# Performance work log

Measured on AMD Instinct MI355X. Metric: run time of the kernel, lower is better.

Reference implementation:

```python
import jax, jax.numpy as jnp
import numpy as np

B, S, E, H, D, RD = 1, 2048, 2560, 32, 80, 32  # batch, seq, n_embd, heads, head_dim, rotary_dim


def setup_inputs() -> dict:
    key = jax.random.key(0)
    k0, k1, k2 = jax.random.split(key, 3)
    hidden_states = jax.random.normal(k0, (B, S, E), dtype=jnp.float32)
    Wqkv_w = jax.random.normal(k1, (3 * E, E), dtype=jnp.float32) * 0.02
    Wqkv_b = jnp.zeros((3 * E,), dtype=jnp.float32)
    out_w = jax.random.normal(k2, (E, E), dtype=jnp.float32) * 0.02
    out_b = jnp.zeros((E,), dtype=jnp.float32)
    # RotaryEmbedding tables: inv_freq over even indices of rotary_dim
    inv_freq = 1.0 / (10000.0 ** (jnp.arange(0, RD, 2, dtype=jnp.float32) / RD))  # [RD/2]
    t = jnp.arange(S, dtype=jnp.float32)
    freqs = t[:, None] * inv_freq[None, :]  # [S, RD/2]
    return {
        "hidden_states": hidden_states,
        "Wqkv_w": Wqkv_w,
        "Wqkv_b": Wqkv_b,
        "out_w": out_w,
        "out_b": out_b,
        "cos": jnp.cos(freqs),
        "sin": jnp.sin(freqs),
    }


def _apply_rotary(x, cos, sin):
    # x: [B, S, H, D]; rotate first 2*cos.shape[-1] dims (GPT-NeoX half-split style)
    rd = cos.shape[-1] * 2
    x_rot, x_pass = x[..., :rd], x[..., rd:]
    x1, x2 = jnp.split(x_rot, 2, axis=-1)
    c = cos[None, :, None, :]  # [1, S, 1, rd/2]
    s = sin[None, :, None, :]
    rotated = jnp.concatenate([x1 * c - x2 * s, x1 * s + x2 * c], axis=-1)
    return jnp.concatenate([rotated, x_pass], axis=-1)


def reference(hidden_states, Wqkv_w, Wqkv_b, out_w, out_b, cos, sin):
    b, s, e = hidden_states.shape
    qkv = hidden_states @ Wqkv_w.T + Wqkv_b              # [B, S, 3E]
    qkv = qkv.reshape(b, s, 3, H, D)
    q = _apply_rotary(qkv[:, :, 0], cos[:s], sin[:s])    # [B, S, H, D]
    k = _apply_rotary(qkv[:, :, 1], cos[:s], sin[:s])
    v = qkv[:, :, 2]
    scale = 1.0 / np.sqrt(D).astype(np.float32)
    scores = jnp.einsum("bthd,bshd->bhts", q, k) * scale  # [B, H, S, S]
    causal = jnp.triu(jnp.full((s, s), -10000.0, dtype=scores.dtype), 1)
    scores = scores + causal
    attn = jax.nn.softmax(scores, axis=-1)
    out = jnp.einsum("bhts,bshd->bthd", attn, v).reshape(b, s, H * D)
    return out @ out_w.T + out_b
```

## Files before the change

kernel.cpp:

```cpp
#include <hip/hip_runtime.h>
#include <hip/hip_bf16.h>

typedef __attribute__((ext_vector_type(8))) __bf16 bf16x8;
typedef __attribute__((ext_vector_type(8))) short s16x8;
typedef __attribute__((ext_vector_type(4))) float f32x4;
typedef unsigned short u16;
typedef unsigned int u32;

static __device__ __forceinline__ float bf2f(u16 u) {
  union { unsigned int i; float f; } x;
  x.i = ((unsigned int)u) << 16;
  return x.f;
}
static __device__ __forceinline__ u16 f2bf(float f) {
  __hip_bfloat16 h = __float2bfloat16(f);
  return __builtin_bit_cast(u16, h);
}

__global__ void cvt_kernel(const float* __restrict__ src, u16* __restrict__ dst, int n4) {
  int stride = gridDim.x * blockDim.x;
  for (int i = blockIdx.x * blockDim.x + threadIdx.x; i < n4; i += stride) {
    float4 f = reinterpret_cast<const float4*>(src)[i];
    ushort4 u;
    u.x = f2bf(f.x); u.y = f2bf(f.y); u.z = f2bf(f.z); u.w = f2bf(f.w);
    reinterpret_cast<ushort4*>(dst)[i] = u;
  }
}

template <typename OUT_T>
__global__ __launch_bounds__(512, 2) void gemm256_bt(
    const u16* __restrict__ A, const u16* __restrict__ B,
    const float* __restrict__ bias, OUT_T* __restrict__ C,
    int M, int N, int K) {
  __shared__ u16 As[2][256 * 64];
  __shared__ u16 Bs[2][256 * 64];
  const int tid = threadIdx.x;
  const int w = tid >> 6;
  const int lane = tid & 63;
  const int g = lane >> 4, c = lane & 15;
  const int wm = w >> 2, wn = w & 3;
  const int nwg = gridDim.x * gridDim.y;
  const int flat = blockIdx.y * gridDim.x + blockIdx.x;
  const int swz = (flat & 7) * (nwg >> 3) + (flat >> 3);
  const int bx = swz % gridDim.x, by = swz / gridDim.x;
  const int row0 = by * 256, col0 = bx * 256;
  const int nt = K >> 6;

  f32x4 acc[8][4] = {};

  auto issue = [&](const u16* __restrict__ base, int rb, int t, u16* lds) {
#pragma unroll
    for (int rr = 0; rr < 4; ++rr) {
      int q = rr * 512 + tid;
      int r = q >> 3;
      int cl = (q & 7) ^ (r & 7);
      const u16* gp = base + (size_t)(rb + r) * K + (t << 6) + cl * 8;
      __builtin_amdgcn_global_load_lds(
          (const __attribute__((address_space(1))) void*)gp,
          (__attribute__((address_space(3))) void*)(lds + q * 8), 16, 0, 0);
    }
  };

  issue(A, row0, 0, As[0]);
  issue(B, col0, 0, Bs[0]);

  int cur = 0;
  for (int t = 0; t < nt; ++t) {
    if (t + 1 < nt) {
      issue(A, row0, t + 1, As[cur ^ 1]);
      issue(B, col0, t + 1, Bs[cur ^ 1]);
      asm volatile("s_waitcnt vmcnt(8)" ::: "memory");
    } else {
      asm volatile("s_waitcnt vmcnt(0)" ::: "memory");
    }
    __builtin_amdgcn_s_barrier();

#pragma unroll
    for (int kk = 0; kk < 2; ++kk) {
      bf16x8 bfr[4], afr[8];
      const int p = (kk * 4 + g) ^ (c & 15 & 7);
#pragma unroll
      for (int nf = 0; nf < 4; ++nf) {
        int rowb = wn * 64 + nf * 16 + c;
        bfr[nf] = *reinterpret_cast<const bf16x8*>(&Bs[cur][(rowb * 8 + p) * 8]);
      }
#pragma unroll
      for (int mf = 0; mf < 8; ++mf) {
        int rowa = wm * 128 + mf * 16 + c;
        afr[mf] = *reinterpret_cast<const bf16x8*>(&As[cur][(rowa * 8 + p) * 8]);
      }
      __builtin_amdgcn_s_setprio(1);
#pragma unroll
      for (int mf = 0; mf < 8; ++mf)
#pragma unroll
        for (int nf = 0; nf < 4; ++nf)
          acc[mf][nf] = __builtin_amdgcn_mfma_f32_16x16x32_bf16(
              afr[mf], bfr[nf], acc[mf][nf], 0, 0, 0);
      __builtin_amdgcn_s_setprio(0);
    }
    __builtin_amdgcn_s_barrier();
    cur ^= 1;
  }

#pragma unroll
  for (int mf = 0; mf < 8; ++mf) {
#pragma unroll
    for (int nf = 0; nf < 4; ++nf) {
      int col = col0 + wn * 64 + nf * 16 + c;
      float bs = bias[col];
#pragma unroll
      for (int r = 0; r < 4; ++r) {
        int row = row0 + wm * 128 + mf * 16 + g * 4 + r;
        float v = acc[mf][nf][r] + bs;
        if constexpr (sizeof(OUT_T) == 2) {
          C[(size_t)row * N + col] = f2bf(v);
        } else {
          C[(size_t)row * N + col] = v;
        }
      }
    }
  }
}

template <typename OUT_T>
__global__ __launch_bounds__(256) void gemm_bt(
    const u16* __restrict__ A, const u16* __restrict__ B,
    const float* __restrict__ bias, OUT_T* __restrict__ C,
    int M, int N, int K) {
  __shared__ u16 As[128 * 64];
  __shared__ u16 Bs[128 * 64];
  const int tid = threadIdx.x;
  const int w = tid >> 6;
  const int lane = tid & 63;
  const int g = lane >> 4;
  const int c = lane & 15;
  const int wm = w >> 1, wn = w & 1;
  const int nwg = gridDim.x * gridDim.y;
  const int flat = blockIdx.y * gridDim.x + blockIdx.x;
  const int swz = (flat & 7) * (nwg >> 3) + (flat >> 3);
  const int bx = swz % gridDim.x, by = swz / gridDim.x;
  const int row0 = by * 128;
  const int col0 = bx * 128;

  f32x4 acc[4][4] = {};

  for (int kt = 0; kt < K; kt += 64) {
    __syncthreads();
#pragma unroll
    for (int i = 0; i < 4; ++i) {
      int q = i * 256 + tid;
      int r = q >> 3;
      int cl = (q & 7) ^ (r & 7);
      const u16* ga = A + (size_t)(row0 + r) * K + kt + cl * 8;
      const u16* gb = B + (size_t)(col0 + r) * K + kt + cl * 8;
      __builtin_amdgcn_global_load_lds(
          (const __attribute__((address_space(1))) void*)ga,
          (__attribute__((address_space(3))) void*)(As + (i * 256 + w * 64) * 8),
          16, 0, 0);
      __builtin_amdgcn_global_load_lds(
          (const __attribute__((address_space(1))) void*)gb,
          (__attribute__((address_space(3))) void*)(Bs + (i * 256 + w * 64) * 8),
          16, 0, 0);
    }
    __syncthreads();
    bf16x8 af[4][2], bf_[4][2];
#pragma unroll
    for (int mi = 0; mi < 4; ++mi)
#pragma unroll
      for (int kk = 0; kk < 2; ++kk) {
        int p = (kk * 4 + g) ^ (c & 7);
        int rowa = wm * 64 + mi * 16 + c;
        int rowb = wn * 64 + mi * 16 + c;
        af[mi][kk] = *reinterpret_cast<const bf16x8*>(&As[(rowa * 8 + p) * 8]);
        bf_[mi][kk] = *reinterpret_cast<const bf16x8*>(&Bs[(rowb * 8 + p) * 8]);
      }
#pragma unroll
    for (int kk = 0; kk < 2; ++kk)
#pragma unroll
      for (int mi = 0; mi < 4; ++mi)
#pragma unroll
        for (int ni = 0; ni < 4; ++ni)
          acc[mi][ni] = __builtin_amdgcn_mfma_f32_16x16x32_bf16(
              af[mi][kk], bf_[ni][kk], acc[mi][ni], 0, 0, 0);
  }

#pragma unroll
  for (int mi = 0; mi < 4; ++mi) {
#pragma unroll
    for (int ni = 0; ni < 4; ++ni) {
      int col = col0 + wn * 64 + ni * 16 + c;
      float bs = bias[col];
#pragma unroll
      for (int r = 0; r < 4; ++r) {
        int row = row0 + wm * 64 + mi * 16 + g * 4 + r;
        float v = acc[mi][ni][r] + bs;
        if constexpr (sizeof(OUT_T) == 2) {
          C[(size_t)row * N + col] = f2bf(v);
        } else {
          C[(size_t)row * N + col] = v;
        }
      }
    }
  }
}

__global__ void rope_kernel(const u16* __restrict__ qkv,
                            const float* __restrict__ cosT,
                            const float* __restrict__ sinT,
                            u16* __restrict__ Qp, u16* __restrict__ Kp) {
  const int s = blockIdx.x;
  const int h = blockIdx.y;
  const int d = threadIdx.x;
  const float scale = 0.16129822f;
  const size_t row = (size_t)s * 7680;
  if (d < 96) {
    float qo = 0.f, ko = 0.f;
    if (d < 80) {
      float q = bf2f(qkv[row + h * 80 + d]);
      float k = bf2f(qkv[row + 2560 + h * 80 + d]);
      if (d < 16) {
        float cs = cosT[s * 16 + d], sn = sinT[s * 16 + d];
        float q2 = bf2f(qkv[row + h * 80 + d + 16]);
        float k2 = bf2f(qkv[row + 2560 + h * 80 + d + 16]);
        qo = q * cs - q2 * sn;
        ko = k * cs - k2 * sn;
      } else if (d < 32) {
        float cs = cosT[s * 16 + d - 16], sn = sinT[s * 16 + d - 16];
        float q1 = bf2f(qkv[row + h * 80 + d - 16]);
        float k1 = bf2f(qkv[row + 2560 + h * 80 + d - 16]);
        qo = q1 * sn + q * cs;
        ko = k1 * sn + k * cs;
      } else {
        qo = q;
        ko = k;
      }
    }
    size_t o = ((size_t)h * 2048 + s) * 96 + d;
    Qp[o] = f2bf(qo * scale);
    Kp[o] = f2bf(ko);
  }
}

__global__ __launch_bounds__(256) void vtrans_kernel(const u16* __restrict__ qkv,
                                                     u16* __restrict__ Vt) {
  __shared__ u16 Vs[80 * 136];
  const int tid = threadIdx.x;
  const int s0 = blockIdx.x * 128;
  const int h = blockIdx.y;
  const int s = tid >> 1;
  const int h2 = tid & 1;
#pragma unroll
  for (int j = 0; j < 5; ++j) {
    s16x8 v = *reinterpret_cast<const s16x8*>(
        &qkv[(size_t)(s0 + s) * 7680 + 5120 + h * 80 + h2 * 40 + j * 8]);
#pragma unroll
    for (int e = 0; e < 8; ++e)
      Vs[(h2 * 40 + j * 8 + e) * 136 + s] = (u16)v[e];
  }
  __syncthreads();
  for (int idx = tid; idx < 80 * 16; idx += 256) {
    int d = idx >> 4, s8 = idx & 15;
    s16x8 v = *reinterpret_cast<const s16x8*>(&Vs[d * 136 + s8 * 8]);
    *reinterpret_cast<s16x8*>(&Vt[((size_t)(h * 80 + d)) * 2048 + s0 + s8 * 8]) = v;
  }
}

__global__ __launch_bounds__(256, 2) void attn_kernel(
    const u16* __restrict__ Qp, const u16* __restrict__ Kp,
    const u16* __restrict__ Vt, u16* __restrict__ O) {
  __shared__ u32 Plds[4][32 * 36];
  __shared__ float mbuf[4][2][16];
  const int tid = threadIdx.x;
  const int w = tid >> 6;
  const int lane = tid & 63;
  const int g = lane >> 4, c = lane & 15;
  const int f = blockIdx.x;
  const int xcd = f & 7;
  const int k_ = f >> 3;
  const int h = (xcd << 2) | (k_ & 3);
  const int qb = 63 - (k_ >> 2);
  const int q0 = qb * 32;
  const size_t hq = (size_t)h * 2048;
  u32* Pw = &Plds[w][0];

  bf16x8 bq[2][3];
#pragma unroll
  for (int qi = 0; qi < 2; ++qi)
#pragma unroll
    for (int ch = 0; ch < 3; ++ch)
      bq[qi][ch] = *reinterpret_cast<const bf16x8*>(
          &Qp[(hq + q0 + qi * 16 + c) * 96 + ch * 32 + g * 8]);

  f32x4 accO[2][5] = {};
  float mrow[2] = {-1e30f, -1e30f};
  float lrow[2] = {0.f, 0.f};

  const int nkb = (q0 + 95) >> 6;
  for (int kbi = w; kbi < nkb; kbi += 4) {
    const int kb = kbi << 6;
    bf16x8 ak[4][3];
#pragma unroll
    for (int ki = 0; ki < 4; ++ki)
#pragma unroll
      for (int ch = 0; ch < 3; ++ch)
        ak[ki][ch] = *reinterpret_cast<const bf16x8*>(
            &Kp[(hq + kb + ki * 16 + c) * 96 + ch * 32 + g * 8]);
    bf16x8 av[5][2];
#pragma unroll
    for (int db = 0; db < 5; ++db)
#pragma unroll
      for (int kc = 0; kc < 2; ++kc)
        av[db][kc] = *reinterpret_cast<const bf16x8*>(
            &Vt[((size_t)h * 80 + db * 16 + c) * 2048 + kb + kc * 32 + g * 8]);

    f32x4 SS[4][2] = {};
    __builtin_amdgcn_s_setprio(1);
#pragma unroll
    for (int ch = 0; ch < 3; ++ch)
#pragma unroll
      for (int ki = 0; ki < 4; ++ki)
#pragma unroll
        for (int qi = 0; qi < 2; ++qi)
          SS[ki][qi] = __builtin_amdgcn_mfma_f32_16x16x32_bf16(
              ak[ki][ch], bq[qi][ch], SS[ki][qi], 0, 0, 0);
    __builtin_amdgcn_s_setprio(0);

    if (kbi == nkb - 1) {
#pragma unroll
      for (int ki = 0; ki < 4; ++ki)
#pragma unroll
        for (int qi = 0; qi < 2; ++qi)
#pragma unroll
          for (int r = 0; r < 4; ++r) {
            int k = kb + ki * 16 + g * 4 + r;
            int q = q0 + qi * 16 + c;
            if (k > q) SS[ki][qi][r] -= 14426.95f;
          }
    }

    float pmax[2];
    bool need = false;
#pragma unroll
    for (int qi = 0; qi < 2; ++qi) {
      float m2 = SS[0][qi][0];
#pragma unroll
      for (int ki = 0; ki < 4; ++ki)
#pragma unroll
        for (int r = 0; r < 4; ++r)
          if (ki | r) m2 = fmaxf(m2, SS[ki][qi][r]);
      m2 = fmaxf(m2, __shfl_xor(m2, 16));
      m2 = fmaxf(m2, __shfl_xor(m2, 32));
      pmax[qi] = m2;
      need = need || (m2 > mrow[qi] + 8.0f);
    }
    if (__any(need)) {
#pragma unroll
      for (int qi = 0; qi < 2; ++qi) {
        float mnew = fmaxf(mrow[qi], pmax[qi]);
        float sc = __builtin_amdgcn_exp2f(mrow[qi] - mnew);
        lrow[qi] *= sc;
#pragma unroll
        for (int db = 0; db < 5; ++db) accO[qi][db] *= sc;
        mrow[qi] = mnew;
      }
    }
#pragma unroll
    for (int qi = 0; qi < 2; ++qi) {
      float rs = 0.f;
#pragma unroll
      for (int ki = 0; ki < 4; ++ki)
#pragma unroll
        for (int r = 0; r < 4; ++r) {
          float pv = __builtin_amdgcn_exp2f(SS[ki][qi][r] - mrow[qi]);
          SS[ki][qi][r] = pv;
          rs += pv;
        }
      rs += __shfl_xor(rs, 16);
      rs += __shfl_xor(rs, 32);
      lrow[qi] += rs;
    }

#pragma unroll
    for (int qi = 0; qi < 2; ++qi)
#pragma unroll
      for (int ki = 0; ki < 4; ++ki)
#pragma unroll
        for (int r2 = 0; r2 < 2; ++r2) {
          u32 lo = f2bf(SS[ki][qi][r2 * 2]);
          u32 hi = f2bf(SS[ki][qi][r2 * 2 + 1]);
          Pw[(qi * 16 + c) * 36 + ki * 8 + g * 2 + r2] = lo | (hi << 16);
        }
    bf16x8 pa[2][2];
#pragma unroll
    for (int qi = 0; qi < 2; ++qi)
#pragma unroll
      for (int kc = 0; kc < 2; ++kc)
        pa[qi][kc] = *reinterpret_cast<const bf16x8*>(
            &Pw[(qi * 16 + c) * 36 + kc * 16 + g * 4]);

    __builtin_amdgcn_s_setprio(1);
#pragma unroll
    for (int kc = 0; kc < 2; ++kc)
#pragma unroll
      for (int db = 0; db < 5; ++db)
#pragma unroll
        for (int qi = 0; qi < 2; ++qi)
          accO[qi][db] = __builtin_amdgcn_mfma_f32_16x16x32_bf16(
              av[db][kc], pa[qi][kc], accO[qi][db], 0, 0, 0);
    __builtin_amdgcn_s_setprio(0);
  }

  mbuf[w][0][c] = mrow[0];
  mbuf[w][1][c] = mrow[1];
  __syncthreads();
#pragma unroll
  for (int qi = 0; qi < 2; ++qi) {
    float ms = fmaxf(fmaxf(mbuf[0][qi][c], mbuf[1][qi][c]),
                     fmaxf(mbuf[2][qi][c], mbuf[3][qi][c]));
    float fl = __builtin_amdgcn_exp2f(mrow[qi] - ms);
    lrow[qi] *= fl;
#pragma unroll
    for (int db = 0; db < 5; ++db) accO[qi][db] *= fl;
  }
  float* mg = (float*)&Plds[0][0] + lane * 44;
  if (w == 0) {
#pragma unroll
    for (int qi = 0; qi < 2; ++qi)
#pragma unroll
      for (int db = 0; db < 5; ++db)
        *reinterpret_cast<f32x4*>(mg + (qi * 5 + db) * 4) = accO[qi][db];
    mg[40] = lrow[0];
    mg[41] = lrow[1];
  }
  __syncthreads();
  if (w == 1) {
#pragma unroll
    for (int qi = 0; qi < 2; ++qi)
#pragma unroll
      for (int db = 0; db < 5; ++db) {
        f32x4 t = *reinterpret_cast<f32x4*>(mg + (qi * 5 + db) * 4);
        *reinterpret_cast<f32x4*>(mg + (qi * 5 + db) * 4) = t + accO[qi][db];
      }
    mg[40] += lrow[0];
    mg[41] += lrow[1];
  }
  __syncthreads();
  if (w == 2) {
#pragma unroll
    for (int qi = 0; qi < 2; ++qi)
#pragma unroll
      for (int db = 0; db < 5; ++db) {
        f32x4 t = *reinterpret_cast<f32x4*>(mg + (qi * 5 + db) * 4);
        *reinterpret_cast<f32x4*>(mg + (qi * 5 + db) * 4) = t + accO[qi][db];
      }
    mg[40] += lrow[0];
    mg[41] += lrow[1];
  }
  __syncthreads();
  if (w == 3) {
    float lf[2];
    lf[0] = 1.0f / (mg[40] + lrow[0]);
    lf[1] = 1.0f / (mg[41] + lrow[1]);
#pragma unroll
    for (int qi = 0; qi < 2; ++qi)
#pragma unroll
      for (int db = 0; db < 5; ++db) {
        f32x4 t = *reinterpret_cast<f32x4*>(mg + (qi * 5 + db) * 4);
        t = t + accO[qi][db];
        ushort4 o4;
        o4.x = f2bf(t[0] * lf[qi]);
        o4.y = f2bf(t[1] * lf[qi]);
        o4.z = f2bf(t[2] * lf[qi]);
        o4.w = f2bf(t[3] * lf[qi]);
        *reinterpret_cast<ushort4*>(
            &O[(size_t)(q0 + qi * 16 + c) * 2560 + h * 80 + db * 16 + g * 4]) = o4;
      }
  }
}

extern "C" void kernel_launch(void* const* d_in, const int* in_sizes, int n_in,
                              void* d_out, int out_size, void* d_ws, size_t ws_size,
                              hipStream_t stream) {
  const float* hs = (const float*)d_in[0];
  const float* Wqkv_w = (const float*)d_in[1];
  const float* Wqkv_b = (const float*)d_in[2];
  const float* out_w = (const float*)d_in[3];
  const float* out_b = (const float*)d_in[4];
  const float* cosT = (const float*)d_in[5];
  const float* sinT = (const float*)d_in[6];
  float* out = (float*)d_out;

  u16* ws = (u16*)d_ws;
  u16* hsb = ws;
  u16* wqkvb = hsb + (size_t)2048 * 2560;
  u16* outwb = wqkvb + (size_t)7680 * 2560;
  u16* qkv = outwb + (size_t)2560 * 2560;
  u16* Qp = qkv + (size_t)2048 * 7680;
  u16* Kp = Qp + (size_t)32 * 2048 * 96;
  u16* Vt = Kp + (size_t)32 * 2048 * 96;
  u16* attn = qkv;

  cvt_kernel<<<dim3(1024), dim3(256), 0, stream>>>(hs, hsb, 5242880 / 4);
  cvt_kernel<<<dim3(2048), dim3(256), 0, stream>>>(Wqkv_w, wqkvb, 19660800 / 4);
  cvt_kernel<<<dim3(1024), dim3(256), 0, stream>>>(out_w, outwb, 6553600 / 4);

  gemm256_bt<u16><<<dim3(30, 8), dim3(512), 0, stream>>>(hsb, wqkvb, Wqkv_b, qkv,
                                                         2048, 7680, 2560);
  rope_kernel<<<dim3(2048, 32), dim3(128), 0, stream>>>(qkv, cosT, sinT, Qp, Kp);
  vtrans_kernel<<<dim3(16, 32), dim3(256), 0, stream>>>(qkv, Vt);
  attn_kernel<<<dim3(2048), dim3(256), 0, stream>>>(Qp, Kp, Vt, attn);
  gemm_bt<float><<<dim3(20, 16), dim3(256), 0, stream>>>(attn, outwb, out_b, out,
                                                         2048, 2560, 2560);
}
```

Baseline: 270.6 us.

## Double-buffer output GEMM, merge convert launches, batch rope rows per block

The output-projection GEMM now uses double-buffered LDS tiles, prefetching the next K tile with async global-to-LDS loads while the current one feeds the MFMAs, with raised wave priority during the MFMA block. The three fp32-to-bf16 conversion launches are merged into one kernel to cut launch overhead. The rope kernel processes 16 sequence rows per 256-thread block instead of one row per 128-thread block, which reduces the block count. The doubled LDS footprint in the GEMM may limit occupancy.

```diff
diff --git a/kernel.cpp b/kernel.cpp
--- a/kernel.cpp
+++ b/kernel.cpp
@@ -17,13 +17,25 @@
   return __builtin_bit_cast(u16, h);
 }
 
-__global__ void cvt_kernel(const float* __restrict__ src, u16* __restrict__ dst, int n4) {
-  int stride = gridDim.x * blockDim.x;
-  for (int i = blockIdx.x * blockDim.x + threadIdx.x; i < n4; i += stride) {
-    float4 f = reinterpret_cast<const float4*>(src)[i];
-    ushort4 u;
-    u.x = f2bf(f.x); u.y = f2bf(f.y); u.z = f2bf(f.z); u.w = f2bf(f.w);
-    reinterpret_cast<ushort4*>(dst)[i] = u;
+__global__ void cvt3_kernel(const float* __restrict__ s0, u16* __restrict__ d0, int n0,
+                            const float* __restrict__ s1, u16* __restrict__ d1, int n1,
+                            const float* __restrict__ s2, u16* __restrict__ d2, int n2) {
+  const int stride = gridDim.x * blockDim.x;
+  const int t0 = blockIdx.x * blockDim.x + threadIdx.x;
+  for (int i = t0; i < n0; i += stride) {
+    float4 f = reinterpret_cast<const float4*>(s0)[i];
+    ushort4 u{f2bf(f.x), f2bf(f.y), f2bf(f.z), f2bf(f.w)};
+    reinterpret_cast<ushort4*>(d0)[i] = u;
+  }
+  for (int i = t0; i < n1; i += stride) {
+    float4 f = reinterpret_cast<const float4*>(s1)[i];
+    ushort4 u{f2bf(f.x), f2bf(f.y), f2bf(f.z), f2bf(f.w)};
+    reinterpret_cast<ushort4*>(d1)[i] = u;
+  }
+  for (int i = t0; i < n2; i += stride) {
+    float4 f = reinterpret_cast<const float4*>(s2)[i];
+    ushort4 u{f2bf(f.x), f2bf(f.y), f2bf(f.z), f2bf(f.w)};
+    reinterpret_cast<ushort4*>(d2)[i] = u;
   }
 }
 
@@ -78,7 +90,7 @@
 #pragma unroll
     for (int kk = 0; kk < 2; ++kk) {
       bf16x8 bfr[4], afr[8];
-      const int p = (kk * 4 + g) ^ (c & 15 & 7);
+      const int p = (kk * 4 + g) ^ (c & 7);
 #pragma unroll
       for (int nf = 0; nf < 4; ++nf) {
         int rowb = wn * 64 + nf * 16 + c;
@@ -123,65 +135,78 @@
 }
 
 template <typename OUT_T>
-__global__ __launch_bounds__(256) void gemm_bt(
+__global__ __launch_bounds__(256, 2) void gemm128p_bt(
     const u16* __restrict__ A, const u16* __restrict__ B,
     const float* __restrict__ bias, OUT_T* __restrict__ C,
     int M, int N, int K) {
-  __shared__ u16 As[128 * 64];
-  __shared__ u16 Bs[128 * 64];
+  __shared__ u16 As[2][128 * 64];
+  __shared__ u16 Bs[2][128 * 64];
   const int tid = threadIdx.x;
   const int w = tid >> 6;
   const int lane = tid & 63;
-  const int g = lane >> 4;
-  const int c = lane & 15;
+  const int g = lane >> 4, c = lane & 15;
   const int wm = w >> 1, wn = w & 1;
   const int nwg = gridDim.x * gridDim.y;
   const int flat = blockIdx.y * gridDim.x + blockIdx.x;
   const int swz = (flat & 7) * (nwg >> 3) + (flat >> 3);
   const int bx = swz % gridDim.x, by = swz / gridDim.x;
-  const int row0 = by * 128;
-  const int col0 = bx * 128;
+  const int row0 = by * 128, col0 = bx * 128;
+  const int nt = K >> 6;
 
   f32x4 acc[4][4] = {};
 
-  for (int kt = 0; kt < K; kt += 64) {
-    __syncthreads();
-#pragma unroll
-    for (int i = 0; i < 4; ++i) {
-      int q = i * 256 + tid;
+  auto issue = [&](const u16* __restrict__ base, int rb, int t, u16* lds) {
+#pragma unroll
+    for (int rr = 0; rr < 4; ++rr) {
+      int q = rr * 256 + tid;
       int r = q >> 3;
       int cl = (q & 7) ^ (r & 7);
-      const u16* ga = A + (size_t)(row0 + r) * K + kt + cl * 8;
-      const u16* gb = B + (size_t)(col0 + r) * K + kt + cl * 8;
+      const u16* gp = base + (size_t)(rb + r) * K + (t << 6) + cl * 8;
       __builtin_amdgcn_global_load_lds(
-          (const __attribute__((address_space(1))) void*)ga,
-          (__attribute__((address_space(3))) void*)(As + (i * 256 + w * 64) * 8),
-          16, 0, 0);
-      __builtin_amdgcn_global_load_lds(
-          (const __attribute__((address_space(1))) void*)gb,
-          (__attribute__((address_space(3))) void*)(Bs + (i * 256 + w * 64) * 8),
-          16, 0, 0);
-    }
-    __syncthreads();
-    bf16x8 af[4][2], bf_[4][2];
-#pragma unroll
-    for (int mi = 0; mi < 4; ++mi)
-#pragma unroll
-      for (int kk = 0; kk < 2; ++kk) {
-        int p = (kk * 4 + g) ^ (c & 7);
+          (const __attribute__((address_space(1))) void*)gp,
+          (__attribute__((address_space(3))) void*)(lds + q * 8), 16, 0, 0);
+    }
+  };
+
+  issue(A, row0, 0, As[0]);
+  issue(B, col0, 0, Bs[0]);
+
+  int cur = 0;
+  for (int t = 0; t < nt; ++t) {
+    if (t + 1 < nt) {
+      issue(A, row0, t + 1, As[cur ^ 1]);
+      issue(B, col0, t + 1, Bs[cur ^ 1]);
+      asm volatile("s_waitcnt vmcnt(8)" ::: "memory");
+    } else {
+      asm volatile("s_waitcnt vmcnt(0)" ::: "memory");
+    }
+    __builtin_amdgcn_s_barrier();
+
+#pragma unroll
+    for (int kk = 0; kk < 2; ++kk) {
+      bf16x8 afr[4], bfr[4];
+      const int p = (kk * 4 + g) ^ (c & 7);
+#pragma unroll
+      for (int mi = 0; mi < 4; ++mi) {
         int rowa = wm * 64 + mi * 16 + c;
-        int rowb = wn * 64 + mi * 16 + c;
-        af[mi][kk] = *reinterpret_cast<const bf16x8*>(&As[(rowa * 8 + p) * 8]);
-        bf_[mi][kk] = *reinterpret_cast<const bf16x8*>(&Bs[(rowb * 8 + p) * 8]);
-      }
-#pragma unroll
-    for (int kk = 0; kk < 2; ++kk)
+        afr[mi] = *reinterpret_cast<const bf16x8*>(&As[cur][(rowa * 8 + p) * 8]);
+      }
+#pragma unroll
+      for (int ni = 0; ni < 4; ++ni) {
+        int rowb = wn * 64 + ni * 16 + c;
+        bfr[ni] = *reinterpret_cast<const bf16x8*>(&Bs[cur][(rowb * 8 + p) * 8]);
+      }
+      __builtin_amdgcn_s_setprio(1);
 #pragma unroll
       for (int mi = 0; mi < 4; ++mi)
 #pragma unroll
         for (int ni = 0; ni < 4; ++ni)
           acc[mi][ni] = __builtin_amdgcn_mfma_f32_16x16x32_bf16(
-              af[mi][kk], bf_[ni][kk], acc[mi][ni], 0, 0, 0);
+              afr[mi], bfr[ni], acc[mi][ni], 0, 0, 0);
+      __builtin_amdgcn_s_setprio(0);
+    }
+    __builtin_amdgcn_s_barrier();
+    cur ^= 1;
   }
 
 #pragma unroll
@@ -204,40 +229,43 @@
   }
 }
 
-__global__ void rope_kernel(const u16* __restrict__ qkv,
-                            const float* __restrict__ cosT,
-                            const float* __restrict__ sinT,
-                            u16* __restrict__ Qp, u16* __restrict__ Kp) {
-  const int s = blockIdx.x;
+__global__ __launch_bounds__(256) void rope_kernel(
+    const u16* __restrict__ qkv, const float* __restrict__ cosT,
+    const float* __restrict__ sinT, u16* __restrict__ Qp, u16* __restrict__ Kp) {
   const int h = blockIdx.y;
-  const int d = threadIdx.x;
+  const int d = threadIdx.x & 127;
+  const int sh = threadIdx.x >> 7;
   const float scale = 0.16129822f;
-  const size_t row = (size_t)s * 7680;
-  if (d < 96) {
-    float qo = 0.f, ko = 0.f;
-    if (d < 80) {
-      float q = bf2f(qkv[row + h * 80 + d]);
-      float k = bf2f(qkv[row + 2560 + h * 80 + d]);
-      if (d < 16) {
-        float cs = cosT[s * 16 + d], sn = sinT[s * 16 + d];
-        float q2 = bf2f(qkv[row + h * 80 + d + 16]);
-        float k2 = bf2f(qkv[row + 2560 + h * 80 + d + 16]);
-        qo = q * cs - q2 * sn;
-        ko = k * cs - k2 * sn;
-      } else if (d < 32) {
-        float cs = cosT[s * 16 + d - 16], sn = sinT[s * 16 + d - 16];
-        float q1 = bf2f(qkv[row + h * 80 + d - 16]);
-        float k1 = bf2f(qkv[row + 2560 + h * 80 + d - 16]);
-        qo = q1 * sn + q * cs;
-        ko = k1 * sn + k * cs;
-      } else {
-        qo = q;
-        ko = k;
-      }
-    }
-    size_t o = ((size_t)h * 2048 + s) * 96 + d;
-    Qp[o] = f2bf(qo * scale);
-    Kp[o] = f2bf(ko);
+#pragma unroll
+  for (int i = 0; i < 8; ++i) {
+    const int s = blockIdx.x * 16 + i * 2 + sh;
+    const size_t row = (size_t)s * 7680;
+    if (d < 96) {
+      float qo = 0.f, ko = 0.f;
+      if (d < 80) {
+        float q = bf2f(qkv[row + h * 80 + d]);
+        float k = bf2f(qkv[row + 2560 + h * 80 + d]);
+        if (d < 16) {
+          float cs = cosT[s * 16 + d], sn = sinT[s * 16 + d];
+          float q2 = bf2f(qkv[row + h * 80 + d + 16]);
+          float k2 = bf2f(qkv[row + 2560 + h * 80 + d + 16]);
+          qo = q * cs - q2 * sn;
+          ko = k * cs - k2 * sn;
+        } else if (d < 32) {
+          float cs = cosT[s * 16 + d - 16], sn = sinT[s * 16 + d - 16];
+          float q1 = bf2f(qkv[row + h * 80 + d - 16]);
+          float k1 = bf2f(qkv[row + 2560 + h * 80 + d - 16]);
+          qo = q1 * sn + q * cs;
+          ko = k1 * sn + k * cs;
+        } else {
+          qo = q;
+          ko = k;
+        }
+      }
+      size_t o = ((size_t)h * 2048 + s) * 96 + d;
+      Qp[o] = f2bf(qo * scale);
+      Kp[o] = f2bf(ko);
+    }
   }
 }
 
@@ -500,15 +528,14 @@
   u16* Vt = Kp + (size_t)32 * 2048 * 96;
   u16* attn = qkv;
 
-  cvt_kernel<<<dim3(1024), dim3(256), 0, stream>>>(hs, hsb, 5242880 / 4);
-  cvt_kernel<<<dim3(2048), dim3(256), 0, stream>>>(Wqkv_w, wqkvb, 19660800 / 4);
-  cvt_kernel<<<dim3(1024), dim3(256), 0, stream>>>(out_w, outwb, 6553600 / 4);
+  cvt3_kernel<<<dim3(2048), dim3(256), 0, stream>>>(
+      hs, hsb, 5242880 / 4, Wqkv_w, wqkvb, 19660800 / 4, out_w, outwb, 6553600 / 4);
 
   gemm256_bt<u16><<<dim3(30, 8), dim3(512), 0, stream>>>(hsb, wqkvb, Wqkv_b, qkv,
                                                          2048, 7680, 2560);
-  rope_kernel<<<dim3(2048, 32), dim3(128), 0, stream>>>(qkv, cosT, sinT, Qp, Kp);
+  rope_kernel<<<dim3(128, 32), dim3(256), 0, stream>>>(qkv, cosT, sinT, Qp, Kp);
   vtrans_kernel<<<dim3(16, 32), dim3(256), 0, stream>>>(qkv, Vt);
   attn_kernel<<<dim3(2048), dim3(256), 0, stream>>>(Qp, Kp, Vt, attn);
-  gemm_bt<float><<<dim3(20, 16), dim3(256), 0, stream>>>(attn, outwb, out_b, out,
-                                                         2048, 2560, 2560);
-}
+  gemm128p_bt<float><<<dim3(20, 16), dim3(256), 0, stream>>>(attn, outwb, out_b, out,
+                                                             2048, 2560, 2560);
+}
```

Measured after the change: 257.5 us. 4.9% less time.
